# Performance work log

Measured on AMD Instinct MI355X. Metric: run time of the kernel, lower is better.

## Reference

```python
import jax, jax.numpy as jnp
import numpy as np

B, T, E = 8, 2048, 1024
H = 16
HD = E // H            # per-head hidden_dim = 64
DFF = 4 * E
DC = T // 512          # decay_constant = 4
EPS = 1e-5


def setup_inputs() -> dict:
    key = jax.random.key(0)
    ks = jax.random.split(key, 8)
    return {
        "x": jax.random.normal(ks[0], (B, T, E), jnp.float32),
        # per-head input projections (Linear(dim, hidden_dim) x H)
        "w_proj": jax.random.normal(ks[1], (H, E, HD), jnp.float32) / np.sqrt(E),
        "b_proj": jnp.zeros((H, HD), jnp.float32),
        # causal mixing weights: first H//2 heads are Col-repeat, last H//2 Row-repeat
        "mix_w": jax.random.normal(ks[2], (H, T), jnp.float32),
        "mix_b": jnp.zeros((H, T), jnp.float32),
        "decay": jnp.ones((H,), jnp.float32),   # decay_value params (init ones as in torch)
        "out_w": jax.random.normal(ks[3], (E, E), jnp.float32) / np.sqrt(E),
        "out_b": jnp.zeros((E,), jnp.float32),
        "ln1_g": jnp.ones((E,), jnp.float32),
        "ln1_b": jnp.zeros((E,), jnp.float32),
        "ln2_g": jnp.ones((E,), jnp.float32),
        "ln2_b": jnp.zeros((E,), jnp.float32),
        "ff_w1": jax.random.normal(ks[4], (E, DFF), jnp.float32) / np.sqrt(E),
        "ff_b1": jnp.zeros((DFF,), jnp.float32),
        "ff_w2": jax.random.normal(ks[5], (DFF, E), jnp.float32) / np.sqrt(DFF),
        "ff_b2": jnp.zeros((E,), jnp.float32),
        "index": 0,
    }


def _layernorm(x, g, b):
    mu = jnp.mean(x, -1, keepdims=True)
    var = jnp.var(x, -1, keepdims=True)
    return (x - mu) * jax.lax.rsqrt(var + EPS) * g + b


def _mix_matrices(mix_w, decay):
    # Col heads: M[i,j] = v[j] * d**((j-i)/DC) for j>=i else 0
    # Row heads: M[i,j] = v[i] * d**((j-i)/DC) for j>=i else 0
    i = jnp.arange(T)[:, None]
    j = jnp.arange(T)[None, :]
    d = jnp.clip(decay, 0.9, 1.0)                                   # (H,)
    expo = (j - i).astype(jnp.float32) / DC                         # (T,T)
    dec = d[:, None, None] ** expo                                  # (H,T,T)
    causal = (j >= i)
    half = H // 2
    Mcol = jnp.where(causal, mix_w[:half, None, :] * dec[:half], 0.0)
    Mrow = jnp.where(causal, mix_w[half:, :, None] * dec[half:], 0.0)
    return jnp.concatenate([Mcol, Mrow], axis=0)                    # (H,T,T)


def reference(x, w_proj, b_proj, mix_w, mix_b, decay, out_w, out_b,
              ln1_g, ln1_b, ln2_g, ln2_b, ff_w1, ff_b1, ff_w2, ff_b2, index):
    # ---- token-mixing sub-block (parallel path of MixedRepeatHeads) ----
    res = x
    h = _layernorm(x, ln1_g, ln1_b)
    # per-head projection: (B,T,E) x (H,E,HD) -> (B,H,T,HD)
    p = jnp.einsum('bte,hef->bhtf', h, w_proj) + b_proj[:, None, :]
    M = _mix_matrices(mix_w, decay)
    # causal decay mixing along time: out[b,h,s,f] = sum_t p[b,h,t,f] * M[h,t,s]
    mixed = jnp.einsum('bhtf,hts->bhsf', p, M) + mix_b[None, :, :, None]
    # concat heads along feature dim -> (B,T,E)
    mixed = mixed.transpose(0, 2, 1, 3).reshape(B, T, E)
    mixed = mixed @ out_w + out_b
    x = mixed + res
    # ---- feed-forward sub-block ----
    res = x
    h = _layernorm(x, ln2_g, ln2_b)
    h = jax.nn.gelu(h @ ff_w1 + ff_b1) @ ff_w2 + ff_b2
    return h + res
```

## Files before the change

### kernel.cpp

```cpp
#include <hip/hip_runtime.h>


#define TT 2048
#define EE 1024
#define HHD 64
#define MROWS 16384
#define SC_L 64

typedef __bf16 bf16x8 __attribute__((ext_vector_type(8)));
typedef float f32x4 __attribute__((ext_vector_type(4)));
typedef unsigned short u16;
typedef unsigned int u32;

__device__ __forceinline__ u16 f2bf(float f) {
  u32 u = __builtin_bit_cast(u32, f);
  u += 0x7FFFu + ((u >> 16) & 1u);
  return (u16)(u >> 16);
}
__device__ __forceinline__ float bf2f(u16 s) {
  u32 u = ((u32)s) << 16;
  return __builtin_bit_cast(float, u);
}
__device__ __forceinline__ float gelu_f(float x) {
  float u = 0.7978845608028654f * x * (1.0f + 0.044715f * x * x);
  float e = __expf(2.0f * u);
  float t = 1.0f - 2.0f / (e + 1.0f);
  return 0.5f * x * (1.0f + t);
}
__device__ __forceinline__ void gload_lds16(const void* g, void* l) {
  __builtin_amdgcn_global_load_lds(
      (const __attribute__((address_space(1))) u32*)g,
      (__attribute__((address_space(3))) u32*)l, 16, 0, 0);
}

__global__ __launch_bounds__(256) void transpose_to_bf16(
    const float* __restrict__ src, u16* __restrict__ dst, int R, int C,
    long sbs, long dbs) {
  __shared__ float tile[32][33];
  src += (long)blockIdx.z * sbs;
  dst += (long)blockIdx.z * dbs;
  int c0 = blockIdx.x * 32, r0 = blockIdx.y * 32;
  int tx = threadIdx.x, ty = threadIdx.y;
#pragma unroll
  for (int i = 0; i < 4; i++)
    tile[ty + i * 8][tx] = src[(long)(r0 + ty + i * 8) * C + c0 + tx];
  __syncthreads();
#pragma unroll
  for (int i = 0; i < 4; i++)
    dst[(long)(c0 + ty + i * 8) * R + r0 + tx] = f2bf(tile[tx][ty + i * 8]);
}

__global__ __launch_bounds__(256) void ln_to_bf16(
    const float* __restrict__ x, const float* __restrict__ gam,
    const float* __restrict__ bet, u16* __restrict__ y) {
  int row = blockIdx.x;
  int tid = threadIdx.x;
  float4 v = ((const float4*)x)[row * 256 + tid];
  float s = v.x + v.y + v.z + v.w;
  float s2 = v.x * v.x + v.y * v.y + v.z * v.z + v.w * v.w;
#pragma unroll
  for (int off = 1; off < 64; off <<= 1) {
    s += __shfl_xor(s, off);
    s2 += __shfl_xor(s2, off);
  }
  __shared__ float red[8];
  int w = tid >> 6;
  if ((tid & 63) == 0) { red[w] = s; red[4 + w] = s2; }
  __syncthreads();
  s = red[0] + red[1] + red[2] + red[3];
  s2 = red[4] + red[5] + red[6] + red[7];
  float mu = s * (1.0f / 1024.0f);
  float var = s2 * (1.0f / 1024.0f) - mu * mu;
  float rstd = rsqrtf(var + 1e-5f);
  int e0 = tid * 4;
  ushort4 o;
  o.x = f2bf((v.x - mu) * rstd * gam[e0 + 0] + bet[e0 + 0]);
  o.y = f2bf((v.y - mu) * rstd * gam[e0 + 1] + bet[e0 + 1]);
  o.z = f2bf((v.z - mu) * rstd * gam[e0 + 2] + bet[e0 + 2]);
  o.w = f2bf((v.w - mu) * rstd * gam[e0 + 3] + bet[e0 + 3]);
  ((ushort4*)y)[row * 256 + tid] = o;
}

template <int EPI>
__global__ __launch_bounds__(512, 2) void gemm256(
    const u16* __restrict__ A, const u16* __restrict__ Bt,
    const float* __restrict__ bias, const float* __restrict__ res, void* outp,
    int M, int N, int K) {
  __shared__ u16 lds[65536];
  const int tid = threadIdx.x;
  const int w = tid >> 6, lane = tid & 63;
  const int wm = w >> 2, wn = w & 3;
  const int l15 = lane & 15, lk = lane >> 4;

  const int gx = (int)gridDim.x;
  const int nwg = gx * (int)gridDim.y;
  const int bid = (int)blockIdx.y * gx + (int)blockIdx.x;
  const int cpx = nwg >> 3;
  const int swz = (bid & 7) * cpx + (bid >> 3);
  const int bx = swz % gx, by = swz / gx;
  const int m0 = by * 256, n0 = bx * 256;

  const int srow = w * 8 + (lane >> 3);
  const int sslot = (lane & 7) ^ (srow & 7);
  const u16* aSrc = A + (size_t)(m0 + srow) * K + sslot * 8;
  const u16* bSrc = Bt + (size_t)(n0 + srow) * K + sslot * 8;
  const size_t rstride = (size_t)64 * K;

  f32x4 acc[8][4];
  const f32x4 z = {0.f, 0.f, 0.f, 0.f};
#pragma unroll
  for (int mi = 0; mi < 8; mi++)
#pragma unroll
    for (int ni = 0; ni < 4; ni++) acc[mi][ni] = z;

  auto STAGE = [&](int c, int kt) {
    const u16* ap = aSrc + kt;
    const u16* bp = bSrc + kt;
    u16* lb = lds + c * 32768 + w * 512;
#pragma unroll
    for (int i = 0; i < 4; i++) {
      gload_lds16(ap + i * rstride, lb + i * 4096);
      gload_lds16(bp + i * rstride, lb + 16384 + i * 4096);
    }
  };

  auto COMPUTE = [&](int c) {
    const bf16x8* Ab = (const bf16x8*)(lds + c * 32768);
    const bf16x8* Bb = (const bf16x8*)(lds + c * 32768 + 16384);
#pragma unroll
    for (int ks = 0; ks < 2; ks++) {
      const int sl = (ks * 4 + lk) ^ (l15 & 7);
      bf16x8 af[8], bv[4];
#pragma unroll
      for (int mi = 0; mi < 8; mi++)
        af[mi] = Ab[(wm * 128 + mi * 16 + l15) * 8 + sl];
#pragma unroll
      for (int ni = 0; ni < 4; ni++)
        bv[ni] = Bb[(wn * 64 + ni * 16 + l15) * 8 + sl];
      __builtin_amdgcn_s_setprio(1);
#pragma unroll
      for (int mi = 0; mi < 8; mi++)
#pragma unroll
        for (int ni = 0; ni < 4; ni++)
          acc[mi][ni] = __builtin_amdgcn_mfma_f32_16x16x32_bf16(af[mi], bv[ni],
                                                                acc[mi][ni], 0, 0, 0);
      __builtin_amdgcn_s_setprio(0);
    }
  };

  const int nt = K >> 6;
  STAGE(0, 0);
  __syncthreads();
  int cur = 0;
  for (int t = 0; t < nt - 1; t++) {
    STAGE(cur ^ 1, (t + 1) << 6);
    COMPUTE(cur);
    __syncthreads();
    cur ^= 1;
  }
  COMPUTE(cur);

#pragma unroll
  for (int mi = 0; mi < 8; mi++) {
#pragma unroll
    for (int ni = 0; ni < 4; ni++) {
      int n = n0 + wn * 64 + ni * 16 + l15;
      float bvv = bias[n];
#pragma unroll
      for (int r = 0; r < 4; r++) {
        int m = m0 + wm * 128 + mi * 16 + lk * 4 + r;
        size_t idx = (size_t)m * N + n;
        float v = acc[mi][ni][r] + bvv;
        if (EPI == 0) {
          ((u16*)outp)[idx] = f2bf(v);
        } else if (EPI == 1) {
          ((float*)outp)[idx] = v + res[idx];
        } else {
          ((u16*)outp)[idx] = f2bf(gelu_f(v));
        }
      }
    }
  }
}

__global__ __launch_bounds__(64) void scan_carry(
    const u16* __restrict__ p, const float* __restrict__ mix_w,
    const float* __restrict__ decay, float* __restrict__ carry) {
  int blk = blockIdx.x;
  int c = blk & 31, h = (blk >> 5) & 15, b = blk >> 9;
  int f = threadIdx.x;
  float d = fminf(fmaxf(decay[h], 0.9f), 1.0f);
  float r = powf(d, 0.25f);
  size_t base = ((size_t)b * TT + c * SC_L) * EE + h * HHD + f;
  const float* mw = mix_w + h * TT + c * SC_L;
  bool isRow = (h >= 8);
  float S = 0.f;
#pragma unroll 4
  for (int t = 0; t < SC_L; t++) {
    float pv = bf2f(p[base + (size_t)t * EE]);
    float q = isRow ? mw[t] * pv : pv;
    S = r * S + q;
  }
  carry[blk * 64 + f] = S;
}

__global__ __launch_bounds__(64) void scan_apply(
    const u16* __restrict__ p, const float* __restrict__ mix_w,
    const float* __restrict__ mix_b, const float* __restrict__ decay,
    const float* __restrict__ carry, u16* __restrict__ mixed) {
  int blk = blockIdx.x;
  int c = blk & 31, h = (blk >> 5) & 15, b = blk >> 9;
  int f = threadIdx.x;
  float d = fminf(fmaxf(decay[h], 0.9f), 1.0f);
  float r = powf(d, 0.25f);
  float rl = powf(r, (float)SC_L);
  int cb = blk - c;
  float S = 0.f;
  for (int cc = 0; cc < c; cc++) S = rl * S + carry[(cb + cc) * 64 + f];
  size_t base = ((size_t)b * TT + c * SC_L) * EE + h * HHD + f;
  const float* mw = mix_w + h * TT + c * SC_L;
  const float* mb = mix_b + h * TT + c * SC_L;
  bool isRow = (h >= 8);
  for (int t = 0; t < SC_L; t++) {
    float pv = bf2f(p[base + (size_t)t * EE]);
    float q = isRow ? mw[t] * pv : pv;
    S = r * S + q;
    float val = (isRow ? S : mw[t] * S) + mb[t];
    mixed[base + (size_t)t * EE] = f2bf(val);
  }
}

extern "C" void kernel_launch(void* const* d_in, const int* in_sizes, int n_in,
                              void* d_out, int out_size, void* d_ws, size_t ws_size,
                              hipStream_t stream) {
  const float* x = (const float*)d_in[0];
  const float* w_proj = (const float*)d_in[1];
  const float* b_proj = (const float*)d_in[2];
  const float* mix_w = (const float*)d_in[3];
  const float* mix_b = (const float*)d_in[4];
  const float* decay = (const float*)d_in[5];
  const float* out_w = (const float*)d_in[6];
  const float* out_b = (const float*)d_in[7];
  const float* ln1_g = (const float*)d_in[8];
  const float* ln1_b = (const float*)d_in[9];
  const float* ln2_g = (const float*)d_in[10];
  const float* ln2_b = (const float*)d_in[11];
  const float* ff_w1 = (const float*)d_in[12];
  const float* ff_b1 = (const float*)d_in[13];
  const float* ff_w2 = (const float*)d_in[14];
  const float* ff_b2 = (const float*)d_in[15];
  float* out = (float*)d_out;

  char* ws = (char*)d_ws;
  const size_t MiB = 1ull << 20;
  u16* wWp = (u16*)(ws + 0 * MiB);
  u16* wWo = (u16*)(ws + 2 * MiB);
  u16* wW1 = (u16*)(ws + 4 * MiB);
  u16* wW2 = (u16*)(ws + 12 * MiB);
  u16* wMix = (u16*)(ws + 20 * MiB);
  u16* wH = (u16*)(ws + 52 * MiB);
  u16* wP = (u16*)(ws + 84 * MiB);
  u16* wU = (u16*)(ws + 52 * MiB);
  float* wCarry = (float*)(ws + 180 * MiB);

  dim3 tb(32, 8);
  transpose_to_bf16<<<dim3(2, 32, 16), tb, 0, stream>>>(w_proj, wWp, 1024, 64,
                                                        65536L, 65536L);
  transpose_to_bf16<<<dim3(32, 32, 1), tb, 0, stream>>>(out_w, wWo, 1024, 1024, 0L, 0L);
  transpose_to_bf16<<<dim3(128, 32, 1), tb, 0, stream>>>(ff_w1, wW1, 1024, 4096, 0L, 0L);
  transpose_to_bf16<<<dim3(32, 128, 1), tb, 0, stream>>>(ff_w2, wW2, 4096, 1024, 0L, 0L);

  ln_to_bf16<<<dim3(MROWS), dim3(256), 0, stream>>>(x, ln1_g, ln1_b, wH);

  gemm256<0><<<dim3(4, 64), dim3(512), 0, stream>>>(
      wH, wWp, b_proj, (const float*)nullptr, (void*)wP, MROWS, 1024, 1024);

  scan_carry<<<dim3(4096), dim3(64), 0, stream>>>(wP, mix_w, decay, wCarry);
  scan_apply<<<dim3(4096), dim3(64), 0, stream>>>(wP, mix_w, mix_b, decay, wCarry, wMix);

  gemm256<1><<<dim3(4, 64), dim3(512), 0, stream>>>(
      wMix, wWo, out_b, x, (void*)out, MROWS, 1024, 1024);

  ln_to_bf16<<<dim3(MROWS), dim3(256), 0, stream>>>(out, ln2_g, ln2_b, wMix);

  gemm256<2><<<dim3(16, 64), dim3(512), 0, stream>>>(
      wMix, wW1, ff_b1, (const float*)nullptr, (void*)wU, MROWS, 4096, 1024);

  gemm256<1><<<dim3(4, 64), dim3(512), 0, stream>>>(
      wU, wW2, ff_b2, out, (void*)out, MROWS, 1024, 4096);
}
```

Baseline: 556.9 us.

## Restructure GEMM main loop into fine-grained interleaved LDS/MFMA phases with k-half staging

The 256x256 bf16 GEMM main loop is rewritten. Each 64-wide K tile is split into two 32-wide halves stored in separate LDS regions with a new 4-slot XOR swizzle. Loads are issued per half, and LDS fragment reads, global-to-LDS staging and MFMA clusters are interleaved in explicit phases separated by s_barrier, sched_barrier and partial vmcnt waits. The goal is to overlap global loads, LDS reads and matrix math more tightly than the old stage-then-compute loop with one sync per tile, and to lower register pressure by holding only 4 A fragments at a time. In exchange there are many more barriers per tile, and the correctness of the hand-placed vmcnt counts becomes fragile.

```diff
diff --git a/kernel.cpp b/kernel.cpp
--- a/kernel.cpp
+++ b/kernel.cpp
@@ -31,6 +31,12 @@
   __builtin_amdgcn_global_load_lds(
       (const __attribute__((address_space(1))) u32*)g,
       (__attribute__((address_space(3))) u32*)l, 16, 0, 0);
+}
+__device__ __forceinline__ void barrier_seq() {
+  asm volatile("" ::: "memory");
+  __builtin_amdgcn_s_barrier();
+  asm volatile("" ::: "memory");
+  __builtin_amdgcn_sched_barrier(0);
 }
 
 __global__ __launch_bounds__(256) void transpose_to_bf16(
@@ -100,11 +106,16 @@
   const int bx = swz % gx, by = swz / gx;
   const int m0 = by * 256, n0 = bx * 256;
 
-  const int srow = w * 8 + (lane >> 3);
-  const int sslot = (lane & 7) ^ (srow & 7);
-  const u16* aSrc = A + (size_t)(m0 + srow) * K + sslot * 8;
-  const u16* bSrc = Bt + (size_t)(n0 + srow) * K + sslot * 8;
-  const size_t rstride = (size_t)64 * K;
+  const int srow = w * 16 + (lane >> 2);
+  const int ssl = ((lane & 3) ^ ((lane >> 2) & 3)) * 8;
+  const u16* aS0 = A + (size_t)(m0 + srow) * K + ssl;
+  const u16* aS1 = A + (size_t)(m0 + 128 + srow) * K + ssl;
+  const u16* bS0 = Bt + (size_t)(n0 + srow) * K + ssl;
+  const u16* bS1 = Bt + (size_t)(n0 + 128 + srow) * K + ssl;
+
+  const int swr = ((lk ^ (l15 & 3)) << 3);
+  const int aBase = (wm * 128 + l15) * 32 + swr;
+  const int bBase = 16384 + (wn * 64 + l15) * 32 + swr;
 
   f32x4 acc[8][4];
   const f32x4 z = {0.f, 0.f, 0.f, 0.f};
@@ -113,52 +124,86 @@
 #pragma unroll
     for (int ni = 0; ni < 4; ni++) acc[mi][ni] = z;
 
-  auto STAGE = [&](int c, int kt) {
-    const u16* ap = aSrc + kt;
-    const u16* bp = bSrc + kt;
-    u16* lb = lds + c * 32768 + w * 512;
-#pragma unroll
-    for (int i = 0; i < 4; i++) {
-      gload_lds16(ap + i * rstride, lb + i * 4096);
-      gload_lds16(bp + i * rstride, lb + 16384 + i * 4096);
-    }
-  };
-
-  auto COMPUTE = [&](int c) {
-    const bf16x8* Ab = (const bf16x8*)(lds + c * 32768);
-    const bf16x8* Bb = (const bf16x8*)(lds + c * 32768 + 16384);
-#pragma unroll
-    for (int ks = 0; ks < 2; ks++) {
-      const int sl = (ks * 4 + lk) ^ (l15 & 7);
-      bf16x8 af[8], bv[4];
-#pragma unroll
-      for (int mi = 0; mi < 8; mi++)
-        af[mi] = Ab[(wm * 128 + mi * 16 + l15) * 8 + sl];
-#pragma unroll
-      for (int ni = 0; ni < 4; ni++)
-        bv[ni] = Bb[(wn * 64 + ni * 16 + l15) * 8 + sl];
-      __builtin_amdgcn_s_setprio(1);
-#pragma unroll
-      for (int mi = 0; mi < 8; mi++)
-#pragma unroll
-        for (int ni = 0; ni < 4; ni++)
-          acc[mi][ni] = __builtin_amdgcn_mfma_f32_16x16x32_bf16(af[mi], bv[ni],
-                                                                acc[mi][ni], 0, 0, 0);
-      __builtin_amdgcn_s_setprio(0);
-    }
-  };
+  bf16x8 a[4], b[4];
+
+#define STAGE_KH(C, KT, KH) { \
+    u16* lb = lds + (C) * 32768 + (KH) * 8192 + w * 512; \
+    const int ko = (KT) + (KH) * 32; \
+    gload_lds16(aS0 + ko, lb); \
+    gload_lds16(aS1 + ko, lb + 4096); \
+    gload_lds16(bS0 + ko, lb + 16384); \
+    gload_lds16(bS1 + ko, lb + 20480); }
+
+#define RD_A(C, KS, CH) { \
+    const u16* lp = lds + (C) * 32768 + (KS) * 8192 + aBase + (CH) * 2048; \
+    a[0] = *(const bf16x8*)(lp); \
+    a[1] = *(const bf16x8*)(lp + 512); \
+    a[2] = *(const bf16x8*)(lp + 1024); \
+    a[3] = *(const bf16x8*)(lp + 1536); }
+
+#define RD_B(C, KS) { \
+    const u16* lp = lds + (C) * 32768 + (KS) * 8192 + bBase; \
+    b[0] = *(const bf16x8*)(lp); \
+    b[1] = *(const bf16x8*)(lp + 512); \
+    b[2] = *(const bf16x8*)(lp + 1024); \
+    b[3] = *(const bf16x8*)(lp + 1536); }
+
+#define MFMA16(CH) { \
+    __builtin_amdgcn_s_setprio(1); \
+    _Pragma("unroll") \
+    for (int mm = 0; mm < 4; mm++) \
+      _Pragma("unroll") \
+      for (int nn = 0; nn < 4; nn++) \
+        acc[(CH) * 4 + mm][nn] = __builtin_amdgcn_mfma_f32_16x16x32_bf16( \
+            a[mm], b[nn], acc[(CH) * 4 + mm][nn], 0, 0, 0); \
+    __builtin_amdgcn_s_setprio(0); }
 
   const int nt = K >> 6;
-  STAGE(0, 0);
-  __syncthreads();
+  STAGE_KH(0, 0, 0);
+  STAGE_KH(0, 0, 1);
+  asm volatile("s_waitcnt vmcnt(0)" ::: "memory");
+  barrier_seq();
+
   int cur = 0;
-  for (int t = 0; t < nt - 1; t++) {
-    STAGE(cur ^ 1, (t + 1) << 6);
-    COMPUTE(cur);
-    __syncthreads();
-    cur ^= 1;
-  }
-  COMPUTE(cur);
+  for (int t = 0; t < nt - 1; ++t) {
+    const int kn = (t + 1) << 6;
+    const int nx = cur ^ 1;
+    RD_A(cur, 0, 0); RD_B(cur, 0);
+    STAGE_KH(nx, kn, 0);
+    barrier_seq();
+    MFMA16(0);
+    barrier_seq();
+    RD_A(cur, 0, 1);
+    STAGE_KH(nx, kn, 1);
+    barrier_seq();
+    MFMA16(1);
+    asm volatile("s_waitcnt vmcnt(8)" ::: "memory");
+    barrier_seq();
+    RD_A(cur, 1, 0); RD_B(cur, 1);
+    barrier_seq();
+    MFMA16(0);
+    barrier_seq();
+    RD_A(cur, 1, 1);
+    barrier_seq();
+    MFMA16(1);
+    asm volatile("s_waitcnt vmcnt(4)" ::: "memory");
+    barrier_seq();
+    cur = nx;
+  }
+  RD_A(cur, 0, 0); RD_B(cur, 0);
+  MFMA16(0);
+  RD_A(cur, 0, 1);
+  MFMA16(1);
+  asm volatile("s_waitcnt vmcnt(0)" ::: "memory");
+  barrier_seq();
+  RD_A(cur, 1, 0); RD_B(cur, 1);
+  MFMA16(0);
+  RD_A(cur, 1, 1);
+  MFMA16(1);
+#undef STAGE_KH
+#undef RD_A
+#undef RD_B
+#undef MFMA16
 
 #pragma unroll
   for (int mi = 0; mi < 8; mi++) {
```

New measurement: 638.8 us. 1.15x slower.

## Restructure GEMM main loop with explicit vmcnt waits and XCD-aware tile mapping

Applied to the files above, without the earlier changes.

The GEMM K-loop now issues the next stage's global-to-LDS loads, then waits with an explicit s_waitcnt vmcnt(8) and raw s_barrier instead of __syncthreads. This lets the in-flight prefetch overlap the current compute. Fragment loads are interleaved per mi row to lower register pressure. Workgroup-to-tile mapping becomes XCD-aware, with per-launch grouping parameters so tiles on the same XCD share A/B panels in L2. GELU is rewritten in the equivalent sigmoid form using a fast reciprocal, and the LDS swizzle slot is simplified.

```diff
diff --git a/kernel.cpp b/kernel.cpp
--- a/kernel.cpp
+++ b/kernel.cpp
@@ -22,15 +22,19 @@
   return __builtin_bit_cast(float, u);
 }
 __device__ __forceinline__ float gelu_f(float x) {
-  float u = 0.7978845608028654f * x * (1.0f + 0.044715f * x * x);
-  float e = __expf(2.0f * u);
-  float t = 1.0f - 2.0f / (e + 1.0f);
-  return 0.5f * x * (1.0f + t);
+  float x2 = x * x;
+  float e = -1.5957691216057308f * x * __builtin_fmaf(0.044715f, x2, 1.0f);
+  return x * __builtin_amdgcn_rcpf(1.0f + __expf(e));
 }
 __device__ __forceinline__ void gload_lds16(const void* g, void* l) {
   __builtin_amdgcn_global_load_lds(
       (const __attribute__((address_space(1))) u32*)g,
       (__attribute__((address_space(3))) u32*)l, 16, 0, 0);
+}
+__device__ __forceinline__ void wg_barrier() {
+  asm volatile("" ::: "memory");
+  __builtin_amdgcn_s_barrier();
+  asm volatile("" ::: "memory");
 }
 
 __global__ __launch_bounds__(256) void transpose_to_bf16(
@@ -85,7 +89,7 @@
 __global__ __launch_bounds__(512, 2) void gemm256(
     const u16* __restrict__ A, const u16* __restrict__ Bt,
     const float* __restrict__ bias, const float* __restrict__ res, void* outp,
-    int M, int N, int K) {
+    int M, int N, int K, int px, int gxp, int byper) {
   __shared__ u16 lds[65536];
   const int tid = threadIdx.x;
   const int w = tid >> 6, lane = tid & 63;
@@ -93,18 +97,17 @@
   const int l15 = lane & 15, lk = lane >> 4;
 
   const int gx = (int)gridDim.x;
-  const int nwg = gx * (int)gridDim.y;
   const int bid = (int)blockIdx.y * gx + (int)blockIdx.x;
-  const int cpx = nwg >> 3;
-  const int swz = (bid & 7) * cpx + (bid >> 3);
-  const int bx = swz % gx, by = swz / gx;
+  const int xcd = bid & 7, i = bid >> 3;
+  const int xg = xcd % gxp, yg = xcd / gxp;
+  const int bx = xg * px + (i % px);
+  const int by = yg * byper + (i / px);
   const int m0 = by * 256, n0 = bx * 256;
 
   const int srow = w * 8 + (lane >> 3);
-  const int sslot = (lane & 7) ^ (srow & 7);
-  const u16* aSrc = A + (size_t)(m0 + srow) * K + sslot * 8;
-  const u16* bSrc = Bt + (size_t)(n0 + srow) * K + sslot * 8;
-  const size_t rstride = (size_t)64 * K;
+  const int sslot = (lane & 7) ^ (lane >> 3);
+  const u16* aS = A + (size_t)(m0 + srow) * K + sslot * 8;
+  const u16* bS = Bt + (size_t)(n0 + srow) * K + sslot * 8;
 
   f32x4 acc[8][4];
   const f32x4 z = {0.f, 0.f, 0.f, 0.f};
@@ -113,52 +116,63 @@
 #pragma unroll
     for (int ni = 0; ni < 4; ni++) acc[mi][ni] = z;
 
-  auto STAGE = [&](int c, int kt) {
-    const u16* ap = aSrc + kt;
-    const u16* bp = bSrc + kt;
-    u16* lb = lds + c * 32768 + w * 512;
-#pragma unroll
-    for (int i = 0; i < 4; i++) {
-      gload_lds16(ap + i * rstride, lb + i * 4096);
-      gload_lds16(bp + i * rstride, lb + 16384 + i * 4096);
+  const int sl0 = (lk ^ (l15 & 7)) * 8;
+  const int sl1 = ((4 + lk) ^ (l15 & 7)) * 8;
+
+#define STAGE_ALL(C, KT) { \
+    u16* lb = lds + (C) * 32768 + w * 512; \
+    gload_lds16(bS + (KT), lb + 16384); \
+    gload_lds16(bS + (size_t)64 * K + (KT), lb + 20480); \
+    gload_lds16(bS + (size_t)128 * K + (KT), lb + 24576); \
+    gload_lds16(bS + (size_t)192 * K + (KT), lb + 28672); \
+    gload_lds16(aS + (KT), lb); \
+    gload_lds16(aS + (size_t)64 * K + (KT), lb + 4096); \
+    gload_lds16(aS + (size_t)128 * K + (KT), lb + 8192); \
+    gload_lds16(aS + (size_t)192 * K + (KT), lb + 12288); }
+
+  const int nt = K >> 6;
+  STAGE_ALL(0, 0);
+
+  for (int t = 0; t < nt; ++t) {
+    const int cur = t & 1, nx = cur ^ 1;
+    if (t + 1 < nt) {
+      STAGE_ALL(nx, (t + 1) << 6);
+      asm volatile("s_waitcnt vmcnt(8)" ::: "memory");
+    } else {
+      asm volatile("s_waitcnt vmcnt(0)" ::: "memory");
     }
-  };
-
-  auto COMPUTE = [&](int c) {
-    const bf16x8* Ab = (const bf16x8*)(lds + c * 32768);
-    const bf16x8* Bb = (const bf16x8*)(lds + c * 32768 + 16384);
-#pragma unroll
-    for (int ks = 0; ks < 2; ks++) {
-      const int sl = (ks * 4 + lk) ^ (l15 & 7);
-      bf16x8 af[8], bv[4];
-#pragma unroll
-      for (int mi = 0; mi < 8; mi++)
-        af[mi] = Ab[(wm * 128 + mi * 16 + l15) * 8 + sl];
+    wg_barrier();
+
+    const u16* lA = lds + cur * 32768;
+    const u16* lB = lA + 16384;
+    bf16x8 bq0[4], bq1[4];
+    {
+      const u16* bp = lB + (wn * 64 + l15) * 64;
+#pragma unroll
+      for (int ni = 0; ni < 4; ni++) {
+        bq0[ni] = *(const bf16x8*)(bp + ni * 1024 + sl0);
+        bq1[ni] = *(const bf16x8*)(bp + ni * 1024 + sl1);
+      }
+    }
+#pragma unroll
+    for (int mi = 0; mi < 8; mi++) {
+      const u16* ap = lA + (wm * 128 + mi * 16 + l15) * 64;
+      bf16x8 a0 = *(const bf16x8*)(ap + sl0);
+      bf16x8 a1 = *(const bf16x8*)(ap + sl1);
+      __builtin_amdgcn_s_setprio(1);
 #pragma unroll
       for (int ni = 0; ni < 4; ni++)
-        bv[ni] = Bb[(wn * 64 + ni * 16 + l15) * 8 + sl];
-      __builtin_amdgcn_s_setprio(1);
-#pragma unroll
-      for (int mi = 0; mi < 8; mi++)
-#pragma unroll
-        for (int ni = 0; ni < 4; ni++)
-          acc[mi][ni] = __builtin_amdgcn_mfma_f32_16x16x32_bf16(af[mi], bv[ni],
-                                                                acc[mi][ni], 0, 0, 0);
+        acc[mi][ni] = __builtin_amdgcn_mfma_f32_16x16x32_bf16(a0, bq0[ni],
+                                                              acc[mi][ni], 0, 0, 0);
+#pragma unroll
+      for (int ni = 0; ni < 4; ni++)
+        acc[mi][ni] = __builtin_amdgcn_mfma_f32_16x16x32_bf16(a1, bq1[ni],
+                                                              acc[mi][ni], 0, 0, 0);
       __builtin_amdgcn_s_setprio(0);
     }
-  };
-
-  const int nt = K >> 6;
-  STAGE(0, 0);
-  __syncthreads();
-  int cur = 0;
-  for (int t = 0; t < nt - 1; t++) {
-    STAGE(cur ^ 1, (t + 1) << 6);
-    COMPUTE(cur);
-    __syncthreads();
-    cur ^= 1;
-  }
-  COMPUTE(cur);
+    wg_barrier();
+  }
+#undef STAGE_ALL
 
 #pragma unroll
   for (int mi = 0; mi < 8; mi++) {
@@ -273,19 +287,23 @@
   ln_to_bf16<<<dim3(MROWS), dim3(256), 0, stream>>>(x, ln1_g, ln1_b, wH);
 
   gemm256<0><<<dim3(4, 64), dim3(512), 0, stream>>>(
-      wH, wWp, b_proj, (const float*)nullptr, (void*)wP, MROWS, 1024, 1024);
+      wH, wWp, b_proj, (const float*)nullptr, (void*)wP, MROWS, 1024, 1024,
+      4, 1, 8);
 
   scan_carry<<<dim3(4096), dim3(64), 0, stream>>>(wP, mix_w, decay, wCarry);
   scan_apply<<<dim3(4096), dim3(64), 0, stream>>>(wP, mix_w, mix_b, decay, wCarry, wMix);
 
   gemm256<1><<<dim3(4, 64), dim3(512), 0, stream>>>(
-      wMix, wWo, out_b, x, (void*)out, MROWS, 1024, 1024);
+      wMix, wWo, out_b, x, (void*)out, MROWS, 1024, 1024,
+      4, 1, 8);
 
   ln_to_bf16<<<dim3(MROWS), dim3(256), 0, stream>>>(out, ln2_g, ln2_b, wMix);
 
   gemm256<2><<<dim3(16, 64), dim3(512), 0, stream>>>(
-      wMix, wW1, ff_b1, (const float*)nullptr, (void*)wU, MROWS, 4096, 1024);
+      wMix, wW1, ff_b1, (const float*)nullptr, (void*)wU, MROWS, 4096, 1024,
+      4, 4, 32);
 
   gemm256<1><<<dim3(4, 64), dim3(512), 0, stream>>>(
-      wU, wW2, ff_b2, out, (void*)out, MROWS, 1024, 4096);
-}
+      wU, wW2, ff_b2, out, (void*)out, MROWS, 1024, 4096,
+      2, 2, 16);
+}
```

New measurement: 551.2 us. No clear change (-1.0%).
